# Optimization experiments

Hardware: AMD Instinct MI355X
Metric: run time of the kernel (lower is better)

## Reference

```python
import jax, jax.numpy as jnp
import numpy as np

N = 100_000      # nodes
E = 1_200_000    # edges per graph (avg degree 12)
D = 64           # args.hidden
PROP_STEP = 8
LAM = 1.0
ALP = 1.0 / (LAM + 1.0)   # args.alp <= 0 -> 1/(lam+1)
LAM0 = 1.0
K = 4
LAM_K = 0.5


def setup_inputs() -> dict:
    key = jax.random.key(0)
    k0, k1, k2, k3, k4 = jax.random.split(key, 5)
    x = jax.random.normal(k0, (N, D), dtype=jnp.float32)
    src0 = jax.random.randint(k1, (E,), 0, N, dtype=jnp.int32)
    # ensure every node has in-degree >= 1 (no isolated dst nodes)
    dst0 = jnp.concatenate([jnp.arange(N, dtype=jnp.int32),
                            jax.random.randint(k2, (E - N,), 0, N, dtype=jnp.int32)])
    src1 = jax.random.randint(k3, (E,), 0, N, dtype=jnp.int32)
    dst1 = jnp.concatenate([jnp.arange(N, dtype=jnp.int32),
                            jax.random.randint(k4, (E - N,), 0, N, dtype=jnp.int32)])
    return {"x": x, "src0": src0, "dst0": dst0, "src1": src1, "dst1": dst1}


def _in_degrees(dst):
    # DGL in_degrees(): count of incoming edges per node
    return jax.ops.segment_sum(jnp.ones(dst.shape, jnp.float32), dst, num_segments=N)


def _normalized_AX(src, dst, inv_sqrt_deg, Y):
    # Y <- D^{-1/2} A D^{-1/2} Y  (edge weight w = 1)
    Yn = Y * inv_sqrt_deg                                    # [N, D]
    agg = jax.ops.segment_sum(Yn[src], dst, num_segments=N)  # gather/scatter SpMM
    return agg * inv_sqrt_deg


def reference(x, src0, dst0, src1, dst1):
    deg0 = _in_degrees(dst0)
    deg1 = _in_degrees(dst1)
    # D^{-1/2} with inf -> 0 (as in D_power_X)
    inv0 = jnp.where(deg0 > 0, deg0 ** -0.5, 0.0)[:, None]
    inv1 = jnp.where(deg1 > 0, deg1 ** -0.5, 0.0)[:, None]
    D0 = deg0[:, None]
    D1 = deg1[:, None]
    Y = x
    for _ in range(PROP_STEP):
        nAX0 = _normalized_AX(src0, dst0, inv0, Y)
        nAX1 = _normalized_AX(src1, dst1, inv1, Y)
        Y = Y - ALP * (LAM0 * (Y - x) / (D0 + D1)
                       + LAM * (Y - nAX0)
                       - (LAM_K / K) * (Y - nAX1))
    return Y
```

## Files before the change

kernel.cpp:

```cpp
#include <hip/hip_runtime.h>
#include <hip/hip_fp16.h>

#define NN 100000
#define NE 1200000
#define DIM 64
#define NBINS 391
#define NBE 128
#define CHUNK (NE / NBE)
#define NBLK ((NN + 255) / 256)



__global__ void __launch_bounds__(256) bin_count(const int* __restrict__ dst0,
                                                 const int* __restrict__ dst1,
                                                 int* __restrict__ blk_cnt) {
    __shared__ int c[NBINS];
    int t = threadIdx.x;
    for (int i = t; i < NBINS; i += 256) c[i] = 0;
    __syncthreads();
    int lo = blockIdx.x * CHUNK, hi = lo + CHUNK;
    for (int e = lo + t; e < hi; e += 256) {
        atomicAdd(&c[dst0[e] >> 8], 1);
        atomicAdd(&c[dst1[e] >> 8], 1);
    }
    __syncthreads();
    for (int i = t; i < NBINS; i += 256) blk_cnt[blockIdx.x * NBINS + i] = c[i];
}

__global__ void __launch_bounds__(512) bin_scan(const int* __restrict__ blk_cnt,
                                                int* __restrict__ bin_start) {
    __shared__ int tot[512];
    int t = threadIdx.x;
    int s = 0;
    if (t < NBINS)
        for (int b = 0; b < NBE; ++b) s += blk_cnt[b * NBINS + t];
    tot[t] = s;
    __syncthreads();
    for (int off = 1; off < 512; off <<= 1) {
        int v = (t >= off) ? tot[t - off] : 0;
        __syncthreads();
        tot[t] += v;
        __syncthreads();
    }
    if (t <= NBINS) bin_start[t] = tot[t] - s;
}

__global__ void __launch_bounds__(NBE) blk_base_k(const int* __restrict__ blk_cnt,
                                                  const int* __restrict__ bin_start,
                                                  int* __restrict__ blk_base) {
    __shared__ int s[NBE];
    int b = blockIdx.x, t = threadIdx.x;
    int v = blk_cnt[t * NBINS + b];
    s[t] = v;
    __syncthreads();
    for (int off = 1; off < NBE; off <<= 1) {
        int x = (t >= off) ? s[t - off] : 0;
        __syncthreads();
        s[t] += x;
        __syncthreads();
    }
    blk_base[t * NBINS + b] = bin_start[b] + s[t] - v;
}

__global__ void __launch_bounds__(256) bin_permute(const int* __restrict__ src0,
                                                   const int* __restrict__ dst0,
                                                   const int* __restrict__ src1,
                                                   const int* __restrict__ dst1,
                                                   const int* __restrict__ blk_base,
                                                   int2* __restrict__ binned) {
    __shared__ int off[NBINS];
    int t = threadIdx.x;
    for (int i = t; i < NBINS; i += 256) off[i] = blk_base[blockIdx.x * NBINS + i];
    __syncthreads();
    int lo = blockIdx.x * CHUNK, hi = lo + CHUNK;
    for (int e = lo + t; e < hi; e += 256) {
        int s = src0[e], d = dst0[e];
        int p = atomicAdd(&off[d >> 8], 1);
        binned[p] = make_int2(s, d);
        s = src1[e]; d = dst1[e];
        p = atomicAdd(&off[d >> 8], 1);
        binned[p] = make_int2(s, d | (1 << 20));
    }
}

__global__ void __launch_bounds__(256) deg_count(const int2* __restrict__ binned,
                                                 const int* __restrict__ bin_start,
                                                 int* __restrict__ deg0,
                                                 int* __restrict__ deg1) {
    __shared__ int dg[512];
    int b = blockIdx.x, t = threadIdx.x;
    dg[t] = 0; dg[t + 256] = 0;
    __syncthreads();
    int lo = bin_start[b], hi = bin_start[b + 1];
    for (int i = lo + t; i < hi; i += 256) {
        int2 r = binned[i];
        int d = r.y & 0xFFFFF, g = r.y >> 20;
        atomicAdd(&dg[((d & 255) << 1) | g], 1);
    }
    __syncthreads();
    int n = b * 256 + t;
    if (n < NN) { deg0[n] = dg[t << 1]; deg1[n] = dg[(t << 1) | 1]; }
}

__global__ void __launch_bounds__(256) scan_l1(const int* __restrict__ deg0,
                                               const int* __restrict__ deg1,
                                               int* __restrict__ rs, int* __restrict__ dp,
                                               int* __restrict__ bs) {
    __shared__ int s0[256];
    int t = threadIdx.x;
    int n = blockIdx.x * 256 + t;
    int a = 0;
    if (n < NN) a = (deg0[n] + deg1[n] + 7) & ~7;
    s0[t] = a;
    __syncthreads();
    for (int off = 1; off < 256; off <<= 1) {
        int x0 = (t >= off) ? s0[t - off] : 0;
        __syncthreads();
        s0[t] += x0;
        __syncthreads();
    }
    if (n < NN) { rs[n] = s0[t] - a; dp[n] = a; }
    if (t == 255) bs[blockIdx.x] = s0[255];
}

__global__ void __launch_bounds__(512) scan_l2(int* __restrict__ bs) {
    __shared__ int s0[512];
    int t = threadIdx.x;
    int a = (t < NBLK) ? bs[t] : 0;
    s0[t] = a;
    __syncthreads();
    for (int off = 1; off < 512; off <<= 1) {
        int x0 = (t >= off) ? s0[t - off] : 0;
        __syncthreads();
        s0[t] += x0;
        __syncthreads();
    }
    if (t < NBLK) bs[t] = s0[t] - a;
}

__global__ void __launch_bounds__(256) scan_l3(int* __restrict__ rs, const int* __restrict__ bs) {
    int n = blockIdx.x * 256 + threadIdx.x;
    if (n < NN) rs[n] += bs[blockIdx.x];
}

__global__ void node_params(const int* __restrict__ deg0, const int* __restrict__ deg1,
                            float* __restrict__ inv0, float* __restrict__ inv1,
                            float2* __restrict__ cf) {
    int n = blockIdx.x * blockDim.x + threadIdx.x;
    if (n < NN) {
        int a = deg0[n], b = deg1[n];
        float i0 = (a > 0) ? rsqrtf((float)a) : 0.0f;
        float i1 = (b > 0) ? rsqrtf((float)b) : 0.0f;
        inv0[n] = i0; inv1[n] = i1;
        int s = a + b;
        float rD = (s > 0) ? 1.0f / (float)s : 0.0f;
        cf[n] = make_float2(0.5625f - 0.5f * rD, 0.5f * rD);
    }
}

__global__ void pad_fill(const int* __restrict__ deg0, const int* __restrict__ deg1,
                         const int* __restrict__ dp, const int* __restrict__ rs,
                         int2* __restrict__ es) {
    int n = blockIdx.x * blockDim.x + threadIdx.x;
    if (n < NN) {
        int b = rs[n] + deg0[n] + deg1[n], e = rs[n] + dp[n];
        for (int i = b; i < e; ++i) es[i] = make_int2(0, 0);
    }
}

__global__ void __launch_bounds__(256) csr_scatter(const int2* __restrict__ binned,
                                                   const int* __restrict__ bin_start,
                                                   const int* __restrict__ rs,
                                                   const float* __restrict__ inv0,
                                                   const float* __restrict__ inv1,
                                                   int2* __restrict__ es) {
    __shared__ int cur[256];
    int b = blockIdx.x, t = threadIdx.x;
    cur[t] = 0;
    __syncthreads();
    int lo = bin_start[b], hi = bin_start[b + 1];
    for (int i = lo + t; i < hi; i += 256) {
        int2 r = binned[i];
        int sN = r.x, d = r.y & 0xFFFFF, g = r.y >> 20;
        float w = g ? (-0.0625f * inv1[d] * inv1[sN]) : (0.5f * inv0[d] * inv0[sN]);
        int p = atomicAdd(&cur[d & 255], 1);
        es[rs[d] + p] = make_int2(sN, __float_as_int(w));
    }
}

__global__ void convert_x(const float* __restrict__ X, __half* __restrict__ Xh) {
    int i = blockIdx.x * blockDim.x + threadIdx.x;
    if (i < NN * DIM / 4) {
        float4 v = ((const float4*)X)[i];
        ushort4 o;
        o.x = __half_as_ushort(__float2half(v.x));
        o.y = __half_as_ushort(__float2half(v.y));
        o.z = __half_as_ushort(__float2half(v.z));
        o.w = __half_as_ushort(__float2half(v.w));
        ((ushort4*)Xh)[i] = o;
    }
}

__global__ void __launch_bounds__(256) step_kernel(
    const float* __restrict__ Yf, const __half* __restrict__ Yh,
    const float* __restrict__ X,
    const int* __restrict__ rs, const int* __restrict__ dp,
    const int2* __restrict__ es, const float2* __restrict__ cf,
    float* __restrict__ Yfo, __half* __restrict__ Yho)
{
    int node = blockIdx.x * 4 + (threadIdx.x >> 6);
    int d = threadIdx.x & 63;
    int un = __builtin_amdgcn_readfirstlane(node);
    int s  = __builtin_amdgcn_readfirstlane(rs[un]);
    int c  = __builtin_amdgcn_readfirstlane(dp[un]);

    float acc = 0.0f;
    int2 eb[8];
#pragma unroll
    for (int k = 0; k < 8; ++k) eb[k] = es[s + k];
    for (int i = 0; i < c; i += 8) {
        int2 en[8];
#pragma unroll
        for (int k = 0; k < 8; ++k) en[k] = es[s + i + 8 + k];
        float yv[8];
#pragma unroll
        for (int k = 0; k < 8; ++k) yv[k] = __half2float(Yh[(size_t)eb[k].x * DIM + d]);
#pragma unroll
        for (int k = 0; k < 8; ++k) acc = fmaf(yv[k], __int_as_float(eb[k].y), acc);
#pragma unroll
        for (int k = 0; k < 8; ++k) eb[k] = en[k];
    }
    float2 cc = cf[un];
    float y  = Yf[(size_t)un * DIM + d];
    float xx = X[(size_t)un * DIM + d];
    float o = cc.x * y + cc.y * xx + acc;
    Yfo[(size_t)un * DIM + d] = o;
    if (Yho) Yho[(size_t)un * DIM + d] = __float2half(o);
}

extern "C" void kernel_launch(void* const* d_in, const int* in_sizes, int n_in,
                              void* d_out, int out_size, void* d_ws, size_t ws_size,
                              hipStream_t stream) {
    const float* x   = (const float*)d_in[0];
    const int* src0  = (const int*)d_in[1];
    const int* dst0  = (const int*)d_in[2];
    const int* src1  = (const int*)d_in[3];
    const int* dst1  = (const int*)d_in[4];
    float* out = (float*)d_out;

    char* ws = (char*)d_ws;
    size_t off = 0;
    auto alloc = [&](size_t bytes) -> void* {
        void* p = ws + off;
        off += (bytes + 255) & ~(size_t)255;
        return p;
    };

    const size_t ES_CAP = (size_t)2 * NE + 8 * NN + 64;

    float*  W    = (float*)alloc((size_t)NN * DIM * 4);
    __half* HA   = (__half*)alloc((size_t)NN * DIM * 2);
    __half* HB   = (__half*)alloc((size_t)NN * DIM * 2);
    int2*   es   = (int2*)alloc(ES_CAP * 8);
    int*    blk_cnt  = (int*)alloc((size_t)NBE * NBINS * 4);
    int*    blk_base = (int*)alloc((size_t)NBE * NBINS * 4);
    int*    bin_st   = (int*)alloc((size_t)(NBINS + 1) * 4);
    int*    deg0 = (int*)alloc((size_t)NN * 4);
    int*    deg1 = (int*)alloc((size_t)NN * 4);
    int*    rs   = (int*)alloc((size_t)NN * 4);
    int*    dp   = (int*)alloc((size_t)NN * 4);
    float*  inv0 = (float*)alloc((size_t)NN * 4);
    float*  inv1 = (float*)alloc((size_t)NN * 4);
    float2* cf   = (float2*)alloc((size_t)NN * 8);
    int*    bs   = (int*)alloc((size_t)NBLK * 4);

    int2* binned = (int2*)W;

    const int TB = 256;
    bin_count<<<NBE, 256, 0, stream>>>(dst0, dst1, blk_cnt);
    bin_scan<<<1, 512, 0, stream>>>(blk_cnt, bin_st);
    blk_base_k<<<NBINS, NBE, 0, stream>>>(blk_cnt, bin_st, blk_base);
    bin_permute<<<NBE, 256, 0, stream>>>(src0, dst0, src1, dst1, blk_base, binned);
    deg_count<<<NBINS, 256, 0, stream>>>(binned, bin_st, deg0, deg1);
    scan_l1<<<NBLK, 256, 0, stream>>>(deg0, deg1, rs, dp, bs);
    scan_l2<<<1, 512, 0, stream>>>(bs);
    scan_l3<<<NBLK, 256, 0, stream>>>(rs, bs);
    node_params<<<(NN + TB - 1) / TB, TB, 0, stream>>>(deg0, deg1, inv0, inv1, cf);
    pad_fill<<<(NN + TB - 1) / TB, TB, 0, stream>>>(deg0, deg1, dp, rs, es);
    csr_scatter<<<NBINS, 256, 0, stream>>>(binned, bin_st, rs, inv0, inv1, es);
    convert_x<<<(NN * DIM / 4 + TB - 1) / TB, TB, 0, stream>>>(x, HA);

    int grid = NN / 4;
    const float* curF = x;
    for (int i = 0; i < 8; ++i) {
        float*  dstF = (i & 1) ? out : W;
        const __half* hin = (i & 1) ? HB : HA;
        __half* hout = (i == 7) ? (__half*)nullptr : ((i & 1) ? HA : HB);
        step_kernel<<<grid, TB, 0, stream>>>(curF, hin, x, rs, dp, es, cf, dstF, hout);
        curF = dstF;
    }
}
```

Before: 548.5 us.

## Pack edges into 4-byte words and keep the propagation state in fp16 only

Edge entries shrink from int2 (source index plus precomputed weight) to a single int that packs the source id, the graph bit and the source degree. The weight is rebuilt in the step kernel from a shared-memory rsqrt table and per-node scale factors. Each step now reads Y and a precomputed fp16 copy of x scaled by the per-node coefficient, instead of fp32 Y and fp32 x, and writes fp32 only on the final step. The CSR scatter sorts edges by source range over several phases, which should improve gather locality. The cost is accumulated fp16 rounding across all 8 steps, an extra lookup and select per edge, and degree values limited to below 128 by the lookup table size.

```diff
diff --git a/kernel.cpp b/kernel.cpp
--- a/kernel.cpp
+++ b/kernel.cpp
@@ -8,7 +8,7 @@
 #define NBE 128
 #define CHUNK (NE / NBE)
 #define NBLK ((NN + 255) / 256)
-
+#define NPH 7
 
 
 __global__ void __launch_bounds__(256) bin_count(const int* __restrict__ dst0,
@@ -144,98 +144,119 @@
 }
 
 __global__ void node_params(const int* __restrict__ deg0, const int* __restrict__ deg1,
-                            float* __restrict__ inv0, float* __restrict__ inv1,
-                            float2* __restrict__ cf) {
+                            float2* __restrict__ nsc, float* __restrict__ sc,
+                            float* __restrict__ cy) {
     int n = blockIdx.x * blockDim.x + threadIdx.x;
     if (n < NN) {
         int a = deg0[n], b = deg1[n];
-        float i0 = (a > 0) ? rsqrtf((float)a) : 0.0f;
-        float i1 = (b > 0) ? rsqrtf((float)b) : 0.0f;
-        inv0[n] = i0; inv1[n] = i1;
+        nsc[n] = make_float2((a > 0) ? 0.5f * rsqrtf((float)a) : 0.0f,
+                             (b > 0) ? -0.0625f * rsqrtf((float)b) : 0.0f);
         int s = a + b;
         float rD = (s > 0) ? 1.0f / (float)s : 0.0f;
-        cf[n] = make_float2(0.5625f - 0.5f * rD, 0.5f * rD);
+        sc[n] = 0.5625f - 0.5f * rD;
+        cy[n] = 0.5f * rD;
     }
 }
 
 __global__ void pad_fill(const int* __restrict__ deg0, const int* __restrict__ deg1,
                          const int* __restrict__ dp, const int* __restrict__ rs,
-                         int2* __restrict__ es) {
+                         int* __restrict__ es) {
     int n = blockIdx.x * blockDim.x + threadIdx.x;
     if (n < NN) {
         int b = rs[n] + deg0[n] + deg1[n], e = rs[n] + dp[n];
-        for (int i = b; i < e; ++i) es[i] = make_int2(0, 0);
+        for (int i = b; i < e; ++i) es[i] = 0;
     }
 }
 
 __global__ void __launch_bounds__(256) csr_scatter(const int2* __restrict__ binned,
                                                    const int* __restrict__ bin_start,
                                                    const int* __restrict__ rs,
-                                                   const float* __restrict__ inv0,
-                                                   const float* __restrict__ inv1,
-                                                   int2* __restrict__ es) {
+                                                   const int* __restrict__ deg0,
+                                                   const int* __restrict__ deg1,
+                                                   int* __restrict__ es) {
     __shared__ int cur[256];
     int b = blockIdx.x, t = threadIdx.x;
     cur[t] = 0;
     __syncthreads();
     int lo = bin_start[b], hi = bin_start[b + 1];
-    for (int i = lo + t; i < hi; i += 256) {
-        int2 r = binned[i];
-        int sN = r.x, d = r.y & 0xFFFFF, g = r.y >> 20;
-        float w = g ? (-0.0625f * inv1[d] * inv1[sN]) : (0.5f * inv0[d] * inv0[sN]);
-        int p = atomicAdd(&cur[d & 255], 1);
-        es[rs[d] + p] = make_int2(sN, __float_as_int(w));
-    }
-}
-
-__global__ void convert_x(const float* __restrict__ X, __half* __restrict__ Xh) {
+    for (int ph = 0; ph < NPH; ++ph) {
+        for (int i = lo + t; i < hi; i += 256) {
+            int2 r = binned[i];
+            int sN = r.x;
+            if ((sN >> 14) != ph) continue;
+            int d = r.y & 0xFFFFF, g = r.y >> 20;
+            int dg = g ? deg1[sN] : deg0[sN];
+            int p = atomicAdd(&cur[d & 255], 1);
+            es[rs[d] + p] = sN | (g << 17) | (dg << 18);
+        }
+        __syncthreads();
+    }
+}
+
+__global__ void convert_x(const float* __restrict__ X, const float* __restrict__ cy,
+                          __half* __restrict__ HA, __half* __restrict__ BX) {
     int i = blockIdx.x * blockDim.x + threadIdx.x;
     if (i < NN * DIM / 4) {
         float4 v = ((const float4*)X)[i];
-        ushort4 o;
-        o.x = __half_as_ushort(__float2half(v.x));
-        o.y = __half_as_ushort(__float2half(v.y));
-        o.z = __half_as_ushort(__float2half(v.z));
-        o.w = __half_as_ushort(__float2half(v.w));
-        ((ushort4*)Xh)[i] = o;
+        float c = cy[i >> 4];
+        ushort4 a, b;
+        a.x = __half_as_ushort(__float2half(v.x));
+        a.y = __half_as_ushort(__float2half(v.y));
+        a.z = __half_as_ushort(__float2half(v.z));
+        a.w = __half_as_ushort(__float2half(v.w));
+        b.x = __half_as_ushort(__float2half(v.x * c));
+        b.y = __half_as_ushort(__float2half(v.y * c));
+        b.z = __half_as_ushort(__float2half(v.z * c));
+        b.w = __half_as_ushort(__float2half(v.w * c));
+        ((ushort4*)HA)[i] = a;
+        ((ushort4*)BX)[i] = b;
     }
 }
 
 __global__ void __launch_bounds__(256) step_kernel(
-    const float* __restrict__ Yf, const __half* __restrict__ Yh,
-    const float* __restrict__ X,
+    const __half* __restrict__ Yh, const __half* __restrict__ BX,
     const int* __restrict__ rs, const int* __restrict__ dp,
-    const int2* __restrict__ es, const float2* __restrict__ cf,
-    float* __restrict__ Yfo, __half* __restrict__ Yho)
+    const int* __restrict__ es, const float2* __restrict__ nsc,
+    const float* __restrict__ sc,
+    __half* __restrict__ Yho, float* __restrict__ Ffo)
 {
+    __shared__ float lut[128];
+    for (int i = threadIdx.x; i < 128; i += 256)
+        lut[i] = (i == 0) ? 0.0f : rsqrtf((float)i);
+    __syncthreads();
+
     int node = blockIdx.x * 4 + (threadIdx.x >> 6);
     int d = threadIdx.x & 63;
     int un = __builtin_amdgcn_readfirstlane(node);
     int s  = __builtin_amdgcn_readfirstlane(rs[un]);
     int c  = __builtin_amdgcn_readfirstlane(dp[un]);
+    float2 ns = nsc[un];
 
     float acc = 0.0f;
-    int2 eb[8];
+    int eb[8];
 #pragma unroll
     for (int k = 0; k < 8; ++k) eb[k] = es[s + k];
     for (int i = 0; i < c; i += 8) {
-        int2 en[8];
+        int en[8];
 #pragma unroll
         for (int k = 0; k < 8; ++k) en[k] = es[s + i + 8 + k];
         float yv[8];
 #pragma unroll
-        for (int k = 0; k < 8; ++k) yv[k] = __half2float(Yh[(size_t)eb[k].x * DIM + d]);
-#pragma unroll
-        for (int k = 0; k < 8; ++k) acc = fmaf(yv[k], __int_as_float(eb[k].y), acc);
+        for (int k = 0; k < 8; ++k)
+            yv[k] = __half2float(Yh[(size_t)(eb[k] & 0x1FFFF) * DIM + d]);
+#pragma unroll
+        for (int k = 0; k < 8; ++k) {
+            float wsc = (eb[k] & (1 << 17)) ? ns.y : ns.x;
+            acc = fmaf(yv[k], wsc * lut[eb[k] >> 18], acc);
+        }
 #pragma unroll
         for (int k = 0; k < 8; ++k) eb[k] = en[k];
     }
-    float2 cc = cf[un];
-    float y  = Yf[(size_t)un * DIM + d];
-    float xx = X[(size_t)un * DIM + d];
-    float o = cc.x * y + cc.y * xx + acc;
-    Yfo[(size_t)un * DIM + d] = o;
-    if (Yho) Yho[(size_t)un * DIM + d] = __float2half(o);
+    float y  = __half2float(Yh[(size_t)un * DIM + d]);
+    float bx = __half2float(BX[(size_t)un * DIM + d]);
+    float o = fmaf(sc[un], y, bx) + acc;
+    if (Ffo) Ffo[(size_t)un * DIM + d] = o;
+    else     Yho[(size_t)un * DIM + d] = __float2half(o);
 }
 
 extern "C" void kernel_launch(void* const* d_in, const int* in_sizes, int n_in,
@@ -258,10 +279,11 @@
 
     const size_t ES_CAP = (size_t)2 * NE + 8 * NN + 64;
 
-    float*  W    = (float*)alloc((size_t)NN * DIM * 4);
     __half* HA   = (__half*)alloc((size_t)NN * DIM * 2);
     __half* HB   = (__half*)alloc((size_t)NN * DIM * 2);
-    int2*   es   = (int2*)alloc(ES_CAP * 8);
+    __half* BX   = (__half*)alloc((size_t)NN * DIM * 2);
+    int2*   binned = (int2*)alloc((size_t)2 * NE * 8);
+    int*    es   = (int*)alloc(ES_CAP * 4);
     int*    blk_cnt  = (int*)alloc((size_t)NBE * NBINS * 4);
     int*    blk_base = (int*)alloc((size_t)NBE * NBINS * 4);
     int*    bin_st   = (int*)alloc((size_t)(NBINS + 1) * 4);
@@ -269,12 +291,10 @@
     int*    deg1 = (int*)alloc((size_t)NN * 4);
     int*    rs   = (int*)alloc((size_t)NN * 4);
     int*    dp   = (int*)alloc((size_t)NN * 4);
-    float*  inv0 = (float*)alloc((size_t)NN * 4);
-    float*  inv1 = (float*)alloc((size_t)NN * 4);
-    float2* cf   = (float2*)alloc((size_t)NN * 8);
+    float2* nsc  = (float2*)alloc((size_t)NN * 8);
+    float*  sc   = (float*)alloc((size_t)NN * 4);
+    float*  cy   = (float*)alloc((size_t)NN * 4);
     int*    bs   = (int*)alloc((size_t)NBLK * 4);
-
-    int2* binned = (int2*)W;
 
     const int TB = 256;
     bin_count<<<NBE, 256, 0, stream>>>(dst0, dst1, blk_cnt);
@@ -285,18 +305,16 @@
     scan_l1<<<NBLK, 256, 0, stream>>>(deg0, deg1, rs, dp, bs);
     scan_l2<<<1, 512, 0, stream>>>(bs);
     scan_l3<<<NBLK, 256, 0, stream>>>(rs, bs);
-    node_params<<<(NN + TB - 1) / TB, TB, 0, stream>>>(deg0, deg1, inv0, inv1, cf);
+    node_params<<<(NN + TB - 1) / TB, TB, 0, stream>>>(deg0, deg1, nsc, sc, cy);
     pad_fill<<<(NN + TB - 1) / TB, TB, 0, stream>>>(deg0, deg1, dp, rs, es);
-    csr_scatter<<<NBINS, 256, 0, stream>>>(binned, bin_st, rs, inv0, inv1, es);
-    convert_x<<<(NN * DIM / 4 + TB - 1) / TB, TB, 0, stream>>>(x, HA);
+    csr_scatter<<<NBINS, 256, 0, stream>>>(binned, bin_st, rs, deg0, deg1, es);
+    convert_x<<<(NN * DIM / 4 + TB - 1) / TB, TB, 0, stream>>>(x, cy, HA, BX);
 
     int grid = NN / 4;
-    const float* curF = x;
     for (int i = 0; i < 8; ++i) {
-        float*  dstF = (i & 1) ? out : W;
         const __half* hin = (i & 1) ? HB : HA;
-        __half* hout = (i == 7) ? (__half*)nullptr : ((i & 1) ? HA : HB);
-        step_kernel<<<grid, TB, 0, stream>>>(curF, hin, x, rs, dp, es, cf, dstF, hout);
-        curF = dstF;
-    }
-}
+        __half* hout = (i & 1) ? HA : HB;
+        float* fout = (i == 7) ? out : nullptr;
+        step_kernel<<<grid, TB, 0, stream>>>(hin, BX, rs, dp, es, nsc, sc, hout, fout);
+    }
+}
```

Result: slower. 608.6 us (+11.0%).
